# Optimization experiments

Hardware: AMD Instinct MI355X
Metric: run time of the kernel (lower is better)

The kernel has to match this reference:

```python
import jax, jax.numpy as jnp
import numpy as np

S, I, C_M, C_P, C_Z = 128, 384, 256, 32, 128

def setup_inputs() -> dict:
    key = jax.random.key(0)
    ks = jax.random.split(key, 7)
    sc = 1.0 / np.sqrt(C_M)
    return {
        "msa_rep": jax.random.normal(ks[0], (S, I, C_M), jnp.float32),
        "ln_gamma": jnp.ones((C_M,), jnp.float32),
        "ln_beta": jnp.zeros((C_M,), jnp.float32),
        "Wa": jax.random.normal(ks[1], (C_P, C_M), jnp.float32) * sc,
        "Wb": jax.random.normal(ks[2], (C_P, C_M), jnp.float32) * sc,
        "Wproj": jax.random.normal(ks[3], (C_Z, C_P * C_P), jnp.float32) / np.sqrt(C_P * C_P),
        "bproj": jnp.zeros((C_Z,), jnp.float32),
    }

def reference(msa_rep, ln_gamma, ln_beta, Wa, Wb, Wproj, bproj):
    # LayerNorm over last dim (eps matches torch default 1e-5)
    mu = jnp.mean(msa_rep, axis=-1, keepdims=True)
    var = jnp.mean(jnp.square(msa_rep - mu), axis=-1, keepdims=True)
    x = (msa_rep - mu) * jax.lax.rsqrt(var + 1e-5) * ln_gamma + ln_beta
    # Two linear projections (torch Linear: y = x @ W.T), no bias
    a = jnp.einsum('sic,pc->sip', x, Wa)  # [s, i, c_p]
    b = jnp.einsum('sic,pc->sip', x, Wb)  # [s, i, c_p]
    norm = 1.0 / msa_rep.shape[-3]
    # Outer product mean over sequences s -> [i, j, c, d]
    outer = norm * jnp.einsum('sic,sjd->ijcd', a, b)
    outer = outer.reshape(outer.shape[0], outer.shape[1], -1)  # [i, j, c*c]
    return jnp.einsum('ijk,zk->ijz', outer, Wproj) + bproj  # [i, j, c_z]
```

## Files before the change

### kernel.cpp

```cpp
#include <hip/hip_runtime.h>
#include <hip/hip_bf16.h>

typedef short s8v   __attribute__((ext_vector_type(8)));
typedef float f32x4 __attribute__((ext_vector_type(4)));
typedef float f32x16 __attribute__((ext_vector_type(16)));

__device__ __forceinline__ unsigned short f2bf(float f) {
  unsigned int b = __float_as_uint(f);
  b += 0x7fffu + ((b >> 16) & 1u);
  return (unsigned short)(b >> 16);
}

__global__ __launch_bounds__(256) void prep_w_kernel(
    const float* __restrict__ Wa, const float* __restrict__ Wb,
    const float* __restrict__ Wproj,
    unsigned short* __restrict__ wab, unsigned short* __restrict__ wfrag) {
  int gid = blockIdx.x * 256 + threadIdx.x;
  if (gid < 16384) {
    int e = gid;
    int j = e & 7, lane = (e >> 3) & 63, kt = (e >> 9) & 7, nt = e >> 12;
    int p = nt * 16 + (lane & 15);
    int c = kt * 32 + ((lane >> 4) << 3) + j;
    float v = (p < 32) ? Wa[p * 256 + c] : Wb[(p - 32) * 256 + c];
    wab[e] = f2bf(v);
  } else {
    int e = gid - 16384;
    int j = e & 7, lane = (e >> 3) & 63, kt2 = (e >> 9) & 63, zt = e >> 15;
    int z = zt * 32 + (lane & 31);
    int kpp = kt2 * 16 + ((lane >> 5) << 3) + j;
    int d = kpp >> 5, c = kpp & 31;
    wfrag[e] = f2bf(Wproj[z * 1024 + c * 32 + d]);
  }
}

#define XS 264
#define OS 66
__global__ __launch_bounds__(256) void kernel_a(
    const float* __restrict__ msa, const float* __restrict__ gamma, const float* __restrict__ beta,
    const unsigned short* __restrict__ wab,
    unsigned short* __restrict__ afrag, unsigned short* __restrict__ bfrag) {
  __shared__ unsigned short xs[64 * XS];
  __shared__ float os[64 * OS];
  const int i  = blockIdx.x >> 1;
  const int sh = blockIdx.x & 1;
  const int tid = threadIdx.x;
  const int w = tid >> 6, lane = tid & 63;
  const int gq = lane >> 4, nlo = lane & 15;

  const float4 g4  = *(const float4*)(gamma + lane * 4);
  const float4 be4 = *(const float4*)(beta  + lane * 4);

  for (int it = 0; it < 16; ++it) {
    const int sl = it * 4 + w;
    const int s  = sh * 64 + sl;
    const float4 v = *(const float4*)(msa + (size_t)(s * 384 + i) * 256 + lane * 4);
    float sum = v.x + v.y + v.z + v.w;
    float sq  = fmaf(v.x, v.x, fmaf(v.y, v.y, fmaf(v.z, v.z, v.w * v.w)));
#pragma unroll
    for (int off = 32; off >= 1; off >>= 1) {
      sum += __shfl_xor(sum, off);
      sq  += __shfl_xor(sq,  off);
    }
    const float mu   = sum * (1.f / 256.f);
    const float var  = sq * (1.f / 256.f) - mu * mu;
    const float rstd = rsqrtf(var + 1e-5f);
    unsigned int lo = (unsigned int)f2bf((v.x - mu) * rstd * g4.x + be4.x)
                    | ((unsigned int)f2bf((v.y - mu) * rstd * g4.y + be4.y) << 16);
    unsigned int hi = (unsigned int)f2bf((v.z - mu) * rstd * g4.z + be4.z)
                    | ((unsigned int)f2bf((v.w - mu) * rstd * g4.w + be4.w) << 16);
    *(uint2*)&xs[sl * XS + lane * 4] = make_uint2(lo, hi);
  }
  __syncthreads();

  const f32x4 z4 = {0.f, 0.f, 0.f, 0.f};
  f32x4 acc[4];
#pragma unroll
  for (int nt = 0; nt < 4; ++nt) acc[nt] = z4;
  for (int kt = 0; kt < 8; ++kt) {
    const s8v av = *(const s8v*)&xs[(w * 16 + nlo) * XS + kt * 32 + gq * 8];
#pragma unroll
    for (int nt = 0; nt < 4; ++nt) {
      const s8v bv = ((const s8v*)wab)[(nt * 8 + kt) * 64 + lane];
      acc[nt] = __builtin_amdgcn_mfma_f32_16x16x32_bf16(av, bv, acc[nt], 0, 0, 0);
    }
  }
#pragma unroll
  for (int nt = 0; nt < 4; ++nt)
#pragma unroll
    for (int r = 0; r < 4; ++r)
      os[(w * 16 + gq * 4 + r) * OS + nt * 16 + nlo] = acc[nt][r];
  __syncthreads();

#pragma unroll
  for (int q = 0; q < 2; ++q) {
    const int set = q * 256 + tid;
    const int lf  = set & 63;
    const int ktl = (set >> 6) & 3;
    const int mat = set >> 8;
    const int gg  = lf >> 5;
    const int p   = mat * 32 + (lf & 31);
    s8v pk;
#pragma unroll
    for (int j = 0; j < 8; ++j)
      pk[j] = (short)f2bf(os[(ktl * 16 + 8 * gg + j) * OS + p]);
    unsigned short* dst = mat ? bfrag : afrag;
    *(s8v*)(dst + ((size_t)((i * 8 + sh * 4 + ktl) * 64 + lf)) * 8) = pk;
  }
}

#define TSM 1032
__global__ __launch_bounds__(1024, 4) void kernel_main(
    const unsigned short* __restrict__ afrag, const unsigned short* __restrict__ bfrag,
    const unsigned short* __restrict__ wfrag, const float* __restrict__ bproj,
    float* __restrict__ out) {
  extern __shared__ unsigned short t[];
  const int bid = blockIdx.x;
  const int bi = bid / 48, bj = bid % 48;
  const int tid = threadIdx.x;
  const int wave = tid >> 6, lane = tid & 63;
  const int g = lane >> 5, l31 = lane & 31;

  const s8v* ag = (const s8v*)afrag;
  const s8v* bg = (const s8v*)bfrag;
  const s8v* wg = (const s8v*)wfrag;

  {
    const int wm = wave >> 2, wn = wave & 3;
    f32x16 a00 = {}, a01 = {}, a10 = {}, a11 = {};
#pragma unroll 2
    for (int kt = 0; kt < 8; ++kt) {
      const s8v av0 = ag[((bi * 8 + wm * 2 + 0) * 8 + kt) * 64 + lane];
      const s8v av1 = ag[((bi * 8 + wm * 2 + 1) * 8 + kt) * 64 + lane];
      const s8v bv0 = bg[((bj * 8 + wn * 2 + 0) * 8 + kt) * 64 + lane];
      const s8v bv1 = bg[((bj * 8 + wn * 2 + 1) * 8 + kt) * 64 + lane];
      a00 = __builtin_amdgcn_mfma_f32_32x32x16_bf16(av0, bv0, a00, 0, 0, 0);
      a01 = __builtin_amdgcn_mfma_f32_32x32x16_bf16(av0, bv1, a01, 0, 0, 0);
      a10 = __builtin_amdgcn_mfma_f32_32x32x16_bf16(av1, bv0, a10, 0, 0, 0);
      a11 = __builtin_amdgcn_mfma_f32_32x32x16_bf16(av1, bv1, a11, 0, 0, 0);
    }
    const int xr = 8 * (l31 & 3);
#pragma unroll
    for (int mt = 0; mt < 2; ++mt)
#pragma unroll
      for (int nt = 0; nt < 2; ++nt) {
        const f32x16& a = (mt == 0) ? (nt == 0 ? a00 : a01) : (nt == 0 ? a10 : a11);
        const int row_t = (wm * 2 + mt) * 8 + wn * 2 + nt;
#pragma unroll
        for (int q = 0; q < 4; ++q) {
          const int c0 = q * 8 + 4 * g;
          const int hw = l31 * 32 + (c0 ^ xr);
          const unsigned int lo = (unsigned int)f2bf(a[q * 4 + 0] * 0.0078125f)
                                | ((unsigned int)f2bf(a[q * 4 + 1] * 0.0078125f) << 16);
          const unsigned int hi = (unsigned int)f2bf(a[q * 4 + 2] * 0.0078125f)
                                | ((unsigned int)f2bf(a[q * 4 + 3] * 0.0078125f) << 16);
          *(uint2*)&t[row_t * TSM + hw] = make_uint2(lo, hi);
        }
      }
  }
  __syncthreads();

  const int zt = wave & 3, kh = wave >> 2;
  f32x16 p0 = {}, p1 = {};
#pragma unroll 4
  for (int k2 = 0; k2 < 16; ++k2) {
    const int kt2 = kh * 16 + k2;
    const int d = kt2 >> 1;
    const int hwb = d * 32 + ((((kt2 & 1) * 16) + 8 * g) ^ (8 * (d & 3)));
    const s8v wv = wg[((zt * 64 + kt2) * 64 + lane)];
    const s8v a0 = *(const s8v*)&t[l31 * TSM + hwb];
    const s8v a1 = *(const s8v*)&t[(32 + l31) * TSM + hwb];
    p0 = __builtin_amdgcn_mfma_f32_32x32x16_bf16(a0, wv, p0, 0, 0, 0);
    p1 = __builtin_amdgcn_mfma_f32_32x32x16_bf16(a1, wv, p1, 0, 0, 0);
  }
  __syncthreads();

  float* sc = (float*)t;
  if (kh > 0) {
    const int slot = zt * 3 + (kh - 1);
#pragma unroll
    for (int r = 0; r < 16; ++r) {
      sc[((slot * 2 + 0) * 16 + r) * 64 + lane] = p0[r];
      sc[((slot * 2 + 1) * 16 + r) * 64 + lane] = p1[r];
    }
  }
  __syncthreads();
  if (kh == 0) {
#pragma unroll
    for (int s2 = 0; s2 < 3; ++s2) {
      const int slot = zt * 3 + s2;
#pragma unroll
      for (int r = 0; r < 16; ++r) {
        p0[r] += sc[((slot * 2 + 0) * 16 + r) * 64 + lane];
        p1[r] += sc[((slot * 2 + 1) * 16 + r) * 64 + lane];
      }
    }
    const int z = zt * 32 + l31;
    const float bz = bproj[z];
#pragma unroll
    for (int r = 0; r < 16; ++r) {
      {
        const int ij = (r & 3) + 8 * (r >> 2) + 4 * g;
        const int gi = bi * 8 + (ij >> 3), gj = bj * 8 + (ij & 7);
        out[(size_t)(gi * 384 + gj) * 128 + z] = p0[r] + bz;
      }
      {
        const int ij = 32 + (r & 3) + 8 * (r >> 2) + 4 * g;
        const int gi = bi * 8 + (ij >> 3), gj = bj * 8 + (ij & 7);
        out[(size_t)(gi * 384 + gj) * 128 + z] = p1[r] + bz;
      }
    }
  }
}

extern "C" void kernel_launch(void* const* d_in, const int* in_sizes, int n_in,
                              void* d_out, int out_size, void* d_ws, size_t ws_size,
                              hipStream_t stream) {
  const float* msa   = (const float*)d_in[0];
  const float* gam   = (const float*)d_in[1];
  const float* bet   = (const float*)d_in[2];
  const float* Wa    = (const float*)d_in[3];
  const float* Wb    = (const float*)d_in[4];
  const float* Wproj = (const float*)d_in[5];
  const float* bpr   = (const float*)d_in[6];
  float* out = (float*)d_out;

  if (ws_size < 6586368) return;
  unsigned short* afrag = (unsigned short*)d_ws;
  unsigned short* bfrag = afrag + 1572864;
  unsigned short* wab   = bfrag + 1572864;
  unsigned short* wfr   = wab + 16384;

  (void)hipFuncSetAttribute(reinterpret_cast<const void*>(kernel_main),
                            hipFuncAttributeMaxDynamicSharedMemorySize, 64 * TSM * 2);

  prep_w_kernel<<<576, 256, 0, stream>>>(Wa, Wb, Wproj, wab, wfr);
  kernel_a<<<768, 256, 0, stream>>>(msa, gam, bet, wab, afrag, bfrag);
  kernel_main<<<2304, 1024, 64 * TSM * 2, stream>>>(afrag, bfrag, wfr, bpr, out);
}
```

Baseline: 134.8 us.

## Split main kernel into two d-chunks with 512 threads and no k-split reduction

```diff
diff --git a/kernel.cpp b/kernel.cpp
--- a/kernel.cpp
+++ b/kernel.cpp
@@ -9,6 +9,11 @@
   unsigned int b = __float_as_uint(f);
   b += 0x7fffu + ((b >> 16) & 1u);
   return (unsigned short)(b >> 16);
+}
+__device__ __forceinline__ unsigned int cvtpk(float x, float y) {
+  unsigned int r;
+  asm("v_cvt_pk_bf16_f32 %0, %1, %2" : "=v"(r) : "v"(x), "v"(y));
+  return r;
 }
 
 __global__ __launch_bounds__(256) void prep_w_kernel(
@@ -91,25 +96,32 @@
       os[(w * 16 + gq * 4 + r) * OS + nt * 16 + nlo] = acc[nt][r];
   __syncthreads();
 
-#pragma unroll
-  for (int q = 0; q < 2; ++q) {
-    const int set = q * 256 + tid;
-    const int lf  = set & 63;
-    const int ktl = (set >> 6) & 3;
-    const int mat = set >> 8;
-    const int gg  = lf >> 5;
-    const int p   = mat * 32 + (lf & 31);
+  {
+    const int lf = tid & 63, ktl = tid >> 6;
+    const int gg = lf >> 5;
+    const int c  = lf & 31;
     s8v pk;
 #pragma unroll
-    for (int j = 0; j < 8; ++j)
-      pk[j] = (short)f2bf(os[(ktl * 16 + 8 * gg + j) * OS + p]);
-    unsigned short* dst = mat ? bfrag : afrag;
-    *(s8v*)(dst + ((size_t)((i * 8 + sh * 4 + ktl) * 64 + lf)) * 8) = pk;
-  }
-}
-
-#define TSM 1032
-__global__ __launch_bounds__(1024, 4) void kernel_main(
+    for (int j8 = 0; j8 < 8; ++j8)
+      pk[j8] = (short)f2bf(os[(ktl * 16 + 8 * gg + j8) * OS + c] * 0.0078125f);
+    *(s8v*)(afrag + ((size_t)((i * 8 + sh * 4 + ktl) * 64 + lf)) * 8) = pk;
+  }
+  {
+    const int dl = tid & 31, ktl = (tid >> 5) & 3, gg = tid >> 7;
+    const int jl = i & 7, bj = i >> 3;
+    const int nt = dl >> 2;
+    const int l31 = (dl & 3) * 8 + jl;
+    const int lf = gg * 32 + l31;
+    s8v pk;
+#pragma unroll
+    for (int j8 = 0; j8 < 8; ++j8)
+      pk[j8] = (short)f2bf(os[(ktl * 16 + 8 * gg + j8) * OS + 32 + dl]);
+    *(s8v*)(bfrag + ((size_t)(((bj * 8 + nt) * 8 + sh * 4 + ktl) * 64 + lf)) * 8) = pk;
+  }
+}
+
+#define TSC 528
+__global__ __launch_bounds__(512, 4) void kernel_main(
     const unsigned short* __restrict__ afrag, const unsigned short* __restrict__ bfrag,
     const unsigned short* __restrict__ wfrag, const float* __restrict__ bproj,
     float* __restrict__ out) {
@@ -119,96 +131,67 @@
   const int tid = threadIdx.x;
   const int wave = tid >> 6, lane = tid & 63;
   const int g = lane >> 5, l31 = lane & 31;
+  const int jl7 = l31 & 7;
 
   const s8v* ag = (const s8v*)afrag;
   const s8v* bg = (const s8v*)bfrag;
   const s8v* wg = (const s8v*)wfrag;
 
-  {
-    const int wm = wave >> 2, wn = wave & 3;
+  const int wm = wave >> 1, wn = wave & 1;
+  const int zt = wave & 3, mts = wave >> 2;
+
+  f32x16 p = {};
+
+#pragma unroll 1
+  for (int dc = 0; dc < 2; ++dc) {
     f32x16 a00 = {}, a01 = {}, a10 = {}, a11 = {};
 #pragma unroll 2
     for (int kt = 0; kt < 8; ++kt) {
       const s8v av0 = ag[((bi * 8 + wm * 2 + 0) * 8 + kt) * 64 + lane];
       const s8v av1 = ag[((bi * 8 + wm * 2 + 1) * 8 + kt) * 64 + lane];
-      const s8v bv0 = bg[((bj * 8 + wn * 2 + 0) * 8 + kt) * 64 + lane];
-      const s8v bv1 = bg[((bj * 8 + wn * 2 + 1) * 8 + kt) * 64 + lane];
+      const s8v bv0 = bg[(((bj * 8 + dc * 4 + wn * 2 + 0) * 8) + kt) * 64 + lane];
+      const s8v bv1 = bg[(((bj * 8 + dc * 4 + wn * 2 + 1) * 8) + kt) * 64 + lane];
       a00 = __builtin_amdgcn_mfma_f32_32x32x16_bf16(av0, bv0, a00, 0, 0, 0);
       a01 = __builtin_amdgcn_mfma_f32_32x32x16_bf16(av0, bv1, a01, 0, 0, 0);
       a10 = __builtin_amdgcn_mfma_f32_32x32x16_bf16(av1, bv0, a10, 0, 0, 0);
       a11 = __builtin_amdgcn_mfma_f32_32x32x16_bf16(av1, bv1, a11, 0, 0, 0);
     }
-    const int xr = 8 * (l31 & 3);
-#pragma unroll
-    for (int mt = 0; mt < 2; ++mt)
-#pragma unroll
-      for (int nt = 0; nt < 2; ++nt) {
-        const f32x16& a = (mt == 0) ? (nt == 0 ? a00 : a01) : (nt == 0 ? a10 : a11);
-        const int row_t = (wm * 2 + mt) * 8 + wn * 2 + nt;
+
+    if (dc) __syncthreads();
+
+#pragma unroll
+    for (int mta = 0; mta < 2; ++mta)
+#pragma unroll
+      for (int ntb = 0; ntb < 2; ++ntb) {
+        const f32x16& a = (mta == 0) ? (ntb == 0 ? a00 : a01) : (ntb == 0 ? a10 : a11);
+        const int row = ((wm * 2 + mta) * 8) + jl7;
+        const int dlc = (wn * 2 + ntb) * 4 + (l31 >> 3);
 #pragma unroll
         for (int q = 0; q < 4; ++q) {
-          const int c0 = q * 8 + 4 * g;
-          const int hw = l31 * 32 + (c0 ^ xr);
-          const unsigned int lo = (unsigned int)f2bf(a[q * 4 + 0] * 0.0078125f)
-                                | ((unsigned int)f2bf(a[q * 4 + 1] * 0.0078125f) << 16);
-          const unsigned int hi = (unsigned int)f2bf(a[q * 4 + 2] * 0.0078125f)
-                                | ((unsigned int)f2bf(a[q * 4 + 3] * 0.0078125f) << 16);
-          *(uint2*)&t[row_t * TSM + hw] = make_uint2(lo, hi);
+          const int hw = (dlc * 32 + q * 8 + 4 * g) ^ (8 * jl7);
+          const unsigned int lo = cvtpk(a[q * 4 + 0], a[q * 4 + 1]);
+          const unsigned int hi = cvtpk(a[q * 4 + 2], a[q * 4 + 3]);
+          *(uint2*)&t[row * TSC + hw] = make_uint2(lo, hi);
         }
       }
-  }
-  __syncthreads();
-
-  const int zt = wave & 3, kh = wave >> 2;
-  f32x16 p0 = {}, p1 = {};
+    __syncthreads();
+
 #pragma unroll 4
-  for (int k2 = 0; k2 < 16; ++k2) {
-    const int kt2 = kh * 16 + k2;
-    const int d = kt2 >> 1;
-    const int hwb = d * 32 + ((((kt2 & 1) * 16) + 8 * g) ^ (8 * (d & 3)));
-    const s8v wv = wg[((zt * 64 + kt2) * 64 + lane)];
-    const s8v a0 = *(const s8v*)&t[l31 * TSM + hwb];
-    const s8v a1 = *(const s8v*)&t[(32 + l31) * TSM + hwb];
-    p0 = __builtin_amdgcn_mfma_f32_32x32x16_bf16(a0, wv, p0, 0, 0, 0);
-    p1 = __builtin_amdgcn_mfma_f32_32x32x16_bf16(a1, wv, p1, 0, 0, 0);
-  }
-  __syncthreads();
-
-  float* sc = (float*)t;
-  if (kh > 0) {
-    const int slot = zt * 3 + (kh - 1);
-#pragma unroll
-    for (int r = 0; r < 16; ++r) {
-      sc[((slot * 2 + 0) * 16 + r) * 64 + lane] = p0[r];
-      sc[((slot * 2 + 1) * 16 + r) * 64 + lane] = p1[r];
-    }
-  }
-  __syncthreads();
-  if (kh == 0) {
-#pragma unroll
-    for (int s2 = 0; s2 < 3; ++s2) {
-      const int slot = zt * 3 + s2;
-#pragma unroll
-      for (int r = 0; r < 16; ++r) {
-        p0[r] += sc[((slot * 2 + 0) * 16 + r) * 64 + lane];
-        p1[r] += sc[((slot * 2 + 1) * 16 + r) * 64 + lane];
-      }
-    }
-    const int z = zt * 32 + l31;
-    const float bz = bproj[z];
-#pragma unroll
-    for (int r = 0; r < 16; ++r) {
-      {
-        const int ij = (r & 3) + 8 * (r >> 2) + 4 * g;
-        const int gi = bi * 8 + (ij >> 3), gj = bj * 8 + (ij & 7);
-        out[(size_t)(gi * 384 + gj) * 128 + z] = p0[r] + bz;
-      }
-      {
-        const int ij = 32 + (r & 3) + 8 * (r >> 2) + 4 * g;
-        const int gi = bi * 8 + (ij >> 3), gj = bj * 8 + (ij & 7);
-        out[(size_t)(gi * 384 + gj) * 128 + z] = p1[r] + bz;
-      }
-    }
+    for (int ks = 0; ks < 32; ++ks) {
+      const int hwb = (ks * 16 + 8 * g) ^ (8 * jl7);
+      const s8v a2 = *(const s8v*)&t[(mts * 32 + l31) * TSC + hwb];
+      const s8v wv = wg[((zt * 64 + dc * 32 + ks) * 64 + lane)];
+      p = __builtin_amdgcn_mfma_f32_32x32x16_bf16(a2, wv, p, 0, 0, 0);
+    }
+  }
+
+  const int z = zt * 32 + l31;
+  const float bz = bproj[z];
+#pragma unroll
+  for (int r = 0; r < 16; ++r) {
+    const int ij = mts * 32 + (r & 3) + 8 * (r >> 2) + 4 * g;
+    const int gi = bi * 8 + (ij >> 3), gj = bj * 8 + (ij & 7);
+    out[(size_t)(gi * 384 + gj) * 128 + z] = p[r] + bz;
   }
 }
 
@@ -231,9 +214,9 @@
   unsigned short* wfr   = wab + 16384;
 
   (void)hipFuncSetAttribute(reinterpret_cast<const void*>(kernel_main),
-                            hipFuncAttributeMaxDynamicSharedMemorySize, 64 * TSM * 2);
+                            hipFuncAttributeMaxDynamicSharedMemorySize, 64 * TSC * 2);
 
   prep_w_kernel<<<576, 256, 0, stream>>>(Wa, Wb, Wproj, wab, wfr);
   kernel_a<<<768, 256, 0, stream>>>(msa, gam, bet, wab, afrag, bfrag);
-  kernel_main<<<2304, 1024, 64 * TSM * 2, stream>>>(afrag, bfrag, wfr, bpr, out);
-}
+  kernel_main<<<2304, 512, 64 * TSC * 2, stream>>>(afrag, bfrag, wfr, bpr, out);
+}
```

Measured after the change: 130.0 us. 3.5% less time.
